# Kernel tuning notes

Measured on AMD Instinct MI355X. Metric: run time of the kernel, lower is better.

## Reference

```python
import jax, jax.numpy as jnp
import numpy as np
import math
from jax import lax

B, T, D, K, H, MLP_DIM, WIN = 4, 2048, 1024, 64, 4, 4096, 128
KH = K // H          # eigenstates per head
HD = D // H          # attention head dim


def layer_norm(x, g, b, eps=1e-5):
    mu = jnp.mean(x, axis=-1, keepdims=True)
    var = jnp.mean(jnp.square(x - mu), axis=-1, keepdims=True)
    return (x - mu) * lax.rsqrt(var + eps) * g + b


def setup_inputs() -> dict:
    key = jax.random.key(0)
    ks = jax.random.split(key, 16)
    s = 0.02
    # layer_idx=1, n_layers=6 -> depth_ratio=0.2, decay_center=-1.7
    return {
        "x": jax.random.normal(ks[0], (B, T, D), jnp.float32),
        "prev_eigenstates": jax.random.normal(ks[1], (B, T, 2 * K), jnp.float32),
        "norm1_g": jnp.ones((D,), jnp.float32),
        "norm1_b": jnp.zeros((D,), jnp.float32),
        "in_proj_w": jax.random.normal(ks[2], (2 * K, D), jnp.float32) * s,
        "memory_gate": jnp.array(-3.0, jnp.float32),
        "memory_proj_w": jnp.eye(2 * K, dtype=jnp.float32),
        "log_decay": jax.random.uniform(ks[3], (K,), jnp.float32, -2.7, -1.2),
        "frequency": jnp.linspace(0.0, 2 * math.pi * (1 - 1 / K), K, dtype=jnp.float32),
        "coupling": jnp.tile(jnp.eye(KH, dtype=jnp.float32), (H, 1, 1))
                    + 0.01 * jax.random.normal(ks[4], (H, KH, KH), jnp.float32) / math.sqrt(KH),
        "main_gate_w": jax.random.normal(ks[5], (D, D), jnp.float32) * s,
        "main_gate_b": jnp.full((D,), -2.0, jnp.float32),
        "out_proj_w": jax.random.normal(ks[6], (D, 2 * K), jnp.float32) * s,
        "attn_norm_g": jnp.ones((D,), jnp.float32),
        "attn_norm_b": jnp.zeros((D,), jnp.float32),
        "attn_in_w": jax.random.normal(ks[7], (3 * D, D), jnp.float32) * s,
        "attn_in_b": jnp.zeros((3 * D,), jnp.float32),
        "attn_out_w": jax.random.normal(ks[8], (D, D), jnp.float32) * s,
        "attn_out_b": jnp.zeros((D,), jnp.float32),
        "norm2_g": jnp.ones((D,), jnp.float32),
        "norm2_b": jnp.zeros((D,), jnp.float32),
        "mlp_w1": jax.random.normal(ks[9], (MLP_DIM, D), jnp.float32) * s,
        "mlp_b1": jnp.zeros((MLP_DIM,), jnp.float32),
        "mlp_w2": jax.random.normal(ks[10], (D, MLP_DIM), jnp.float32) * s,
        "mlp_b2": jnp.zeros((D,), jnp.float32),
    }


def eigenstate_fft(log_decay, frequency, beta_r, beta_i):
    # diagonal complex SSM recurrence: c_t = lam * c_{t-1} + beta_t
    lam = jnp.exp(log_decay)
    lr = lam * jnp.cos(frequency)   # (K,)
    li = lam * jnp.sin(frequency)
    br = jnp.transpose(beta_r, (1, 0, 2))  # (T,B,K)
    bi = jnp.transpose(beta_i, (1, 0, 2))

    def step(carry, inp):
        sr, si = carry
        xr, xi = inp
        nr = lr * sr - li * si + xr
        ni = lr * si + li * sr + xi
        return (nr, ni), (nr, ni)

    init = (jnp.zeros(br.shape[1:], br.dtype), jnp.zeros(bi.shape[1:], bi.dtype))
    _, (cr, ci) = lax.scan(step, init, (br, bi))
    return jnp.transpose(cr, (1, 0, 2)), jnp.transpose(ci, (1, 0, 2))


def reference(x, prev_eigenstates, norm1_g, norm1_b, in_proj_w, memory_gate,
              memory_proj_w, log_decay, frequency, coupling, main_gate_w,
              main_gate_b, out_proj_w, attn_norm_g, attn_norm_b, attn_in_w,
              attn_in_b, attn_out_w, attn_out_b, norm2_g, norm2_b,
              mlp_w1, mlp_b1, mlp_w2, mlp_b2):
    b, t, d = x.shape
    residual = x
    x_norm = layer_norm(x, norm1_g, norm1_b)

    beta = jnp.einsum('btd,kd->btk', x_norm, in_proj_w)        # (B,T,2K)
    beta_r, beta_i = jnp.split(beta, 2, axis=-1)

    # cross-layer memory
    mg = jax.nn.sigmoid(memory_gate)
    prev = jnp.einsum('btk,jk->btj', prev_eigenstates, memory_proj_w)
    pr, pi = jnp.split(prev, 2, axis=-1)
    beta_r = beta_r + mg * pr
    beta_i = beta_i + mg * pi

    c_r, c_i = eigenstate_fft(log_decay, frequency, beta_r, beta_i)  # (B,T,K)

    # per-head coupling
    c_r_h = c_r.reshape(b, t, H, KH)
    c_i_h = c_i.reshape(b, t, H, KH)
    c_r = jnp.einsum('hjk,bthk->bthj', coupling, c_r_h).reshape(b, t, K)
    c_i = jnp.einsum('hjk,bthk->bthj', coupling, c_i_h).reshape(b, t, K)
    eigenstates_out = jnp.concatenate([c_r, c_i], axis=-1)     # (B,T,2K)

    h = jnp.einsum('btk,dk->btd', eigenstates_out, out_proj_w)
    # spectral gate (band gates computed in torch are unused in the output)
    main_g = jax.nn.sigmoid(jnp.einsum('btd,ed->bte', x_norm, main_gate_w) + main_gate_b)
    h = main_g * h
    x = residual + h

    # sliding-window attention (dense masked MHA, as in the source)
    attn_in = layer_norm(x, attn_norm_g, attn_norm_b)
    qkv = jnp.einsum('btd,ed->bte', attn_in, attn_in_w) + attn_in_b
    q, k_, v = jnp.split(qkv, 3, axis=-1)
    q = q.reshape(b, t, H, HD).transpose(0, 2, 1, 3)           # (B,H,T,hd)
    k_ = k_.reshape(b, t, H, HD).transpose(0, 2, 1, 3)
    v = v.reshape(b, t, H, HD).transpose(0, 2, 1, 3)
    scale = 1.0 / math.sqrt(HD)
    scores = jnp.einsum('bhqd,bhkd->bhqk', q, k_) * scale
    idx = jnp.arange(t)
    diff = idx[:, None] - idx[None, :]
    allowed = (diff >= 0) & (diff <= WIN)                      # True = attend
    scores = jnp.where(allowed, scores, jnp.finfo(scores.dtype).min)
    attn = jax.nn.softmax(scores, axis=-1)
    ao = jnp.einsum('bhqk,bhkd->bhqd', attn, v)
    ao = ao.transpose(0, 2, 1, 3).reshape(b, t, d)
    ao = jnp.einsum('btd,ed->bte', ao, attn_out_w) + attn_out_b
    x = x + ao

    # MLP
    x2 = layer_norm(x, norm2_g, norm2_b)
    m = jax.nn.silu(jnp.einsum('btd,md->btm', x2, mlp_w1) + mlp_b1)
    m = jnp.einsum('btm,dm->btd', m, mlp_w2) + mlp_b2
    x = x + m
    return (x, eigenstates_out)
```

## Files before the change

### kernel.cpp

```cpp
#include <hip/hip_runtime.h>


typedef __bf16 bf16_t;
typedef bf16_t bf16x8 __attribute__((ext_vector_type(8)));
typedef bf16_t bf16x4 __attribute__((ext_vector_type(4)));
typedef float  f32x4  __attribute__((ext_vector_type(4)));

#define Tc   2048
#define Dc   1024
#define BTc  8192
#define K2c  128
#define MLPc 4096

struct ConvSeg { const float* src; bf16_t* dst; int n; };
struct ConvArgs { ConvSeg s[9]; };

__global__ __launch_bounds__(256) void convert_kernel(ConvArgs a) {
    ConvSeg sg = a.s[blockIdx.y];
    int i = (blockIdx.x * 256 + threadIdx.x) * 4;
    if (i >= sg.n) return;
    float4 v = *(const float4*)(sg.src + i);
    bf16x4 o;
    o[0] = (bf16_t)v.x; o[1] = (bf16_t)v.y; o[2] = (bf16_t)v.z; o[3] = (bf16_t)v.w;
    *(bf16x4*)(sg.dst + i) = o;
}

__global__ __launch_bounds__(256) void ln_kernel(const float* __restrict__ x,
                                                 const float* __restrict__ g,
                                                 const float* __restrict__ bb,
                                                 bf16_t* __restrict__ out) {
    int row = blockIdx.x;
    int tid = threadIdx.x;
    float4 v = ((const float4*)(x + (size_t)row * Dc))[tid];
    float s  = v.x + v.y + v.z + v.w;
    float ss = v.x * v.x + v.y * v.y + v.z * v.z + v.w * v.w;
#pragma unroll
    for (int d = 32; d > 0; d >>= 1) {
        s  += __shfl_down(s, d);
        ss += __shfl_down(ss, d);
    }
    __shared__ float red[8];
    int wv = tid >> 6;
    if ((tid & 63) == 0) { red[wv] = s; red[4 + wv] = ss; }
    __syncthreads();
    s  = red[0] + red[1] + red[2] + red[3];
    ss = red[4] + red[5] + red[6] + red[7];
    float mean = s * (1.0f / Dc);
    float var  = ss * (1.0f / Dc) - mean * mean;
    float rstd = rsqrtf(var + 1e-5f);
    float4 g4 = ((const float4*)g)[tid];
    float4 b4 = ((const float4*)bb)[tid];
    bf16x4 o;
    o[0] = (bf16_t)((v.x - mean) * rstd * g4.x + b4.x);
    o[1] = (bf16_t)((v.y - mean) * rstd * g4.y + b4.y);
    o[2] = (bf16_t)((v.z - mean) * rstd * g4.z + b4.z);
    o[3] = (bf16_t)((v.w - mean) * rstd * g4.w + b4.w);
    *(bf16x4*)(out + (size_t)row * Dc + tid * 4) = o;
}

#define BM 128
#define BN 128
#define BK 32

struct EpiParams {
    const float* bias;
    float*       fout;
    const float* fin;
    bf16_t*      bout;
    bf16_t*      q; bf16_t* k; bf16_t* v;
    const float* hbuf;
};

#define GLOAD_LDS(g, l)                                                        \
    __builtin_amdgcn_global_load_lds(                                          \
        (const __attribute__((address_space(1))) unsigned int*)(g),            \
        (__attribute__((address_space(3))) unsigned int*)(l), 16, 0, 0)

template <int EPI>
__global__ __launch_bounds__(256) void gemm_tiled(const bf16_t* __restrict__ A,
                                                  const bf16_t* __restrict__ W,
                                                  int M, int N, int K,
                                                  EpiParams ep) {
    __shared__ bf16_t As[BM * BK];
    __shared__ bf16_t Bs[BN * BK];

    int tid = threadIdx.x;
    int wv = tid >> 6, lane = tid & 63;
    int lane16 = lane & 15, quad = lane >> 4;
    int nbn = N / BN;
    int bm = blockIdx.x / nbn, bn = blockIdx.x % nbn;
    int m0 = bm * BM, n0 = bn * BN;
    int wm = (wv >> 1) * 64, wn = (wv & 1) * 64;

    int lrow = lane >> 2;
    int lcol = (lane & 3) * 8;
    const bf16_t* ga = A + (size_t)(m0 + wv * 16 + lrow) * K + lcol;
    const bf16_t* gb = W + (size_t)(n0 + wv * 16 + lrow) * K + lcol;
    size_t gstep64 = (size_t)64 * K;
    bf16_t* la0 = &As[(wv * 16) * BK];
    bf16_t* la1 = &As[(64 + wv * 16) * BK];
    bf16_t* lb0 = &Bs[(wv * 16) * BK];
    bf16_t* lb1 = &Bs[(64 + wv * 16) * BK];

    f32x4 zz = {0.f, 0.f, 0.f, 0.f};
    f32x4 acc[4][4];
#pragma unroll
    for (int mi = 0; mi < 4; mi++)
#pragma unroll
        for (int ni = 0; ni < 4; ni++) acc[mi][ni] = zz;

    for (int k0 = 0; k0 < K; k0 += BK) {
        GLOAD_LDS(ga + k0, la0);
        GLOAD_LDS(ga + k0 + gstep64, la1);
        GLOAD_LDS(gb + k0, lb0);
        GLOAD_LDS(gb + k0 + gstep64, lb1);
        __syncthreads();
        bf16x8 af[4], bf[4];
#pragma unroll
        for (int mi = 0; mi < 4; mi++)
            af[mi] = *(const bf16x8*)&As[(wm + mi * 16 + lane16) * BK + quad * 8];
#pragma unroll
        for (int ni = 0; ni < 4; ni++)
            bf[ni] = *(const bf16x8*)&Bs[(wn + ni * 16 + lane16) * BK + quad * 8];
#pragma unroll
        for (int mi = 0; mi < 4; mi++)
#pragma unroll
            for (int ni = 0; ni < 4; ni++)
                acc[mi][ni] = __builtin_amdgcn_mfma_f32_16x16x32_bf16(
                    af[mi], bf[ni], acc[mi][ni], 0, 0, 0);
        __syncthreads();
    }

#pragma unroll
    for (int mi = 0; mi < 4; mi++)
#pragma unroll
        for (int ni = 0; ni < 4; ni++)
#pragma unroll
            for (int r = 0; r < 4; r++) {
                int row = m0 + wm + mi * 16 + quad * 4 + r;
                int col = n0 + wn + ni * 16 + lane16;
                float v = acc[mi][ni][r];
                if constexpr (EPI == 0) {
                    ep.fout[(size_t)row * N + col] = v;
                } else if constexpr (EPI == 1) {
                    v += ep.bias[col];
                    ep.bout[(size_t)row * N + col] = (bf16_t)(v / (1.0f + __expf(-v)));
                } else if constexpr (EPI == 2) {
                    size_t o = (size_t)row * N + col;
                    ep.fout[o] = ep.fin[o] + v + ep.bias[col];
                } else if constexpr (EPI == 3) {
                    v += ep.bias[col];
                    int part = col >> 10, d1 = col & 1023;
                    int hh = d1 >> 8, hd = d1 & 255;
                    int b = row >> 11, t = row & 2047;
                    bf16_t* dst = (part == 0) ? ep.q : (part == 1) ? ep.k : ep.v;
                    dst[(((size_t)(b * 4 + hh) * Tc + t) << 8) + hd] = (bf16_t)v;
                } else if constexpr (EPI == 4) {
                    size_t o = (size_t)row * N + col;
                    float g = 1.0f / (1.0f + __expf(-(v + ep.bias[col])));
                    ep.fout[o] = ep.fin[o] + g * ep.hbuf[o];
                }
            }
}

__device__ __forceinline__ void mm32(const bf16_t* __restrict__ A,
                                     const bf16_t* __restrict__ W,
                                     int K, int m0, int n0,
                                     int lane16, int quad, f32x4 (&acc)[2][2]) {
    const bf16_t* a0 = A + (size_t)(m0 + lane16) * K + quad * 8;
    const bf16_t* a1 = a0 + (size_t)16 * K;
    const bf16_t* w0 = W + (size_t)(n0 + lane16) * K + quad * 8;
    const bf16_t* w1 = w0 + (size_t)16 * K;
#pragma unroll 4
    for (int k = 0; k < K; k += 32) {
        bf16x8 av0 = *(const bf16x8*)(a0 + k);
        bf16x8 av1 = *(const bf16x8*)(a1 + k);
        bf16x8 bv0 = *(const bf16x8*)(w0 + k);
        bf16x8 bv1 = *(const bf16x8*)(w1 + k);
        acc[0][0] = __builtin_amdgcn_mfma_f32_16x16x32_bf16(av0, bv0, acc[0][0], 0, 0, 0);
        acc[0][1] = __builtin_amdgcn_mfma_f32_16x16x32_bf16(av0, bv1, acc[0][1], 0, 0, 0);
        acc[1][0] = __builtin_amdgcn_mfma_f32_16x16x32_bf16(av1, bv0, acc[1][0], 0, 0, 0);
        acc[1][1] = __builtin_amdgcn_mfma_f32_16x16x32_bf16(av1, bv1, acc[1][1], 0, 0, 0);
    }
}

__global__ __launch_bounds__(256) void gemm_beta(const bf16_t* __restrict__ xn,
                                                 const bf16_t* __restrict__ ipw,
                                                 const bf16_t* __restrict__ prevb,
                                                 const bf16_t* __restrict__ mpw,
                                                 const float* __restrict__ mgate_p,
                                                 float* __restrict__ beta_c) {
    int lane = threadIdx.x & 63;
    int wave = threadIdx.x >> 6;
    int gid  = blockIdx.x * 4 + wave;
    int mt = gid / 4, nt = gid % 4;
    int m0 = mt * 32, n0 = nt * 32;
    int lane16 = lane & 15, quad = lane >> 4;
    f32x4 zz = {0.f, 0.f, 0.f, 0.f};
    f32x4 acc[2][2] = {{zz, zz}, {zz, zz}};
    mm32(xn, ipw, Dc, m0, n0, lane16, quad, acc);
    f32x4 acc2[2][2] = {{zz, zz}, {zz, zz}};
    mm32(prevb, mpw, K2c, m0, n0, lane16, quad, acc2);
    float mg = 1.0f / (1.0f + __expf(-mgate_p[0]));
    for (int mi = 0; mi < 2; mi++)
        for (int ni = 0; ni < 2; ni++)
            for (int r = 0; r < 4; r++) {
                int row = m0 + mi * 16 + quad * 4 + r;
                int col = n0 + ni * 16 + lane16;
                int b = row >> 11, t = row & 2047;
                beta_c[((size_t)b * K2c + col) * Tc + t] =
                    acc[mi][ni][r] + mg * acc2[mi][ni][r];
            }
}

__global__ __launch_bounds__(64) void scan_kernel(const float* __restrict__ beta_c,
                                                  const float* __restrict__ log_decay,
                                                  const float* __restrict__ freq,
                                                  float* __restrict__ cbuf) {
    int b = blockIdx.x >> 6;
    int k = blockIdx.x & 63;
    int lane = threadIdx.x;
    float lam = expf(log_decay[k]);
    float fr = freq[k];
    float lr = lam * cosf(fr), li = lam * sinf(fr);

    const float* br_p = beta_c + ((size_t)b * K2c + k) * Tc + lane * 32;
    const float* bi_p = beta_c + ((size_t)b * K2c + 64 + k) * Tc + lane * 32;
    float br[32], bi[32];
#pragma unroll
    for (int i = 0; i < 8; i++) {
        *(float4*)(&br[i * 4]) = ((const float4*)br_p)[i];
        *(float4*)(&bi[i * 4]) = ((const float4*)bi_p)[i];
    }
    float sr = 0.f, si = 0.f;
#pragma unroll
    for (int i = 0; i < 32; i++) {
        float nr = lr * sr - li * si + br[i];
        float ni = lr * si + li * sr + bi[i];
        sr = nr; si = ni;
    }
    float Mr = lr, Mi = li;
#pragma unroll
    for (int i = 0; i < 5; i++) {
        float nr = Mr * Mr - Mi * Mi, ni = 2.f * Mr * Mi;
        Mr = nr; Mi = ni;
    }
    float ir = sr, ii = si;
#pragma unroll
    for (int d = 1; d < 64; d <<= 1) {
        float pr = __shfl_up(ir, d);
        float pi = __shfl_up(ii, d);
        if (lane >= d) {
            ir += Mr * pr - Mi * pi;
            ii += Mr * pi + Mi * pr;
        }
        float nr = Mr * Mr - Mi * Mi, ni = 2.f * Mr * Mi;
        Mr = nr; Mi = ni;
    }
    float cr = __shfl_up(ir, 1), ci = __shfl_up(ii, 1);
    if (lane == 0) { cr = 0.f; ci = 0.f; }
    float* cr_p = cbuf + ((size_t)b * K2c + k) * Tc + lane * 32;
    float* ci_p = cbuf + ((size_t)b * K2c + 64 + k) * Tc + lane * 32;
    sr = cr; si = ci;
#pragma unroll
    for (int i = 0; i < 32; i++) {
        float nr = lr * sr - li * si + br[i];
        float ni = lr * si + li * sr + bi[i];
        sr = nr; si = ni;
        cr_p[i] = sr; ci_p[i] = si;
    }
}

__global__ __launch_bounds__(256) void coupling_kernel(const float* __restrict__ cbuf,
                                                       const float* __restrict__ cpl,
                                                       float* __restrict__ eig_out,
                                                       bf16_t* __restrict__ eigb) {
    int idx = blockIdx.x * 256 + threadIdx.x;
    int col = idx & 127;
    int t = (idx >> 7) & 2047;
    int b = idx >> 18;
    int ri = col >> 6, hj = col & 63, h2 = hj >> 4, j = hj & 15;
    const float* crow = cbuf + ((size_t)b * K2c + ri * 64 + h2 * 16) * Tc + t;
    const float* cw = cpl + (h2 * 16 + j) * 16;
    float acc = 0.f;
#pragma unroll
    for (int kk = 0; kk < 16; kk++) acc += cw[kk] * crow[(size_t)kk * Tc];
    eig_out[idx] = acc;
    eigb[idx] = (bf16_t)acc;
}

#define TQ   16
#define NK   144
#define LDQ  264
#define LDKV 136
#define LDS_S 161

__global__ __launch_bounds__(256) void attn_kernel(const bf16_t* __restrict__ qb,
                                                   const bf16_t* __restrict__ kb,
                                                   const bf16_t* __restrict__ vb,
                                                   bf16_t* __restrict__ ao) {
    __shared__ bf16_t Qs[TQ * LDQ];
    __shared__ bf16_t KVs[NK * LDKV];
    __shared__ float  S[TQ * LDS_S];
    __shared__ float  l_l[TQ];

    int tid = threadIdx.x;
    int qt = blockIdx.x & 127;
    int bh = blockIdx.x >> 7;
    int q0 = qt * TQ;
    const bf16_t* qp = qb + (size_t)bh * Tc * 256;
    const bf16_t* kp = kb + (size_t)bh * Tc * 256;
    const bf16_t* vp = vb + (size_t)bh * Tc * 256;

#pragma unroll
    for (int i = 0; i < 2; i++) {
        int lin = tid + i * 256;
        int row = lin >> 5, c = lin & 31;
        uint4 val = *(const uint4*)(qp + (size_t)(q0 + row) * 256 + c * 8);
        *(uint4*)(&Qs[row * LDQ + c * 8]) = val;
    }

    int q = tid >> 4;
    int kk0 = (tid & 15) * 9;
    float s9[9];
#pragma unroll
    for (int j = 0; j < 9; j++) s9[j] = 0.f;

    for (int ph = 0; ph < 2; ph++) {
        __syncthreads();
#pragma unroll
        for (int i = 0; i < 9; i++) {
            int lin = tid + i * 256;
            int row = lin >> 4, c = lin & 15;
            int kg = q0 - 128 + row;
            uint4 val = make_uint4(0u, 0u, 0u, 0u);
            if (kg >= 0) val = *(const uint4*)(kp + (size_t)kg * 256 + ph * 128 + c * 8);
            *(uint4*)(&KVs[row * LDKV + c * 8]) = val;
        }
        __syncthreads();
        for (int dt = 0; dt < 16; dt++) {
            float q8[8];
#pragma unroll
            for (int d = 0; d < 8; d++)
                q8[d] = (float)Qs[q * LDQ + ph * 128 + dt * 8 + d];
#pragma unroll
            for (int j = 0; j < 9; j++) {
                const bf16_t* kr = &KVs[(kk0 + j) * LDKV + dt * 8];
                float a = 0.f;
#pragma unroll
                for (int d = 0; d < 8; d++) a += q8[d] * (float)kr[d];
                s9[j] += a;
            }
        }
    }
#pragma unroll
    for (int j = 0; j < 9; j++) {
        int kk = kk0 + j;
        int kg = q0 - 128 + kk;
        bool ok = (kg >= 0) && (kk >= q) && (kk <= q + 128);
        S[q * LDS_S + kk] = ok ? s9[j] * 0.0625f : -1e30f;
    }
    __syncthreads();
    if (tid < TQ) {
        float m = -1e30f;
        for (int kk = 0; kk < NK; kk++) m = fmaxf(m, S[tid * LDS_S + kk]);
        float l = 0.f;
        for (int kk = 0; kk < NK; kk++) {
            float p = __expf(S[tid * LDS_S + kk] - m);
            S[tid * LDS_S + kk] = p;
            l += p;
        }
        l_l[tid] = l;
    }

    int dq = tid & 15;
    int b = bh >> 2, h = bh & 3;
    for (int ph = 0; ph < 2; ph++) {
        __syncthreads();
#pragma unroll
        for (int i = 0; i < 9; i++) {
            int lin = tid + i * 256;
            int row = lin >> 4, c = lin & 15;
            int kg = q0 - 128 + row;
            uint4 val = make_uint4(0u, 0u, 0u, 0u);
            if (kg >= 0) val = *(const uint4*)(vp + (size_t)kg * 256 + ph * 128 + c * 8);
            *(uint4*)(&KVs[row * LDKV + c * 8]) = val;
        }
        __syncthreads();
        float o[8];
#pragma unroll
        for (int j = 0; j < 8; j++) o[j] = 0.f;
        int d0 = dq * 8;
        for (int kk = 0; kk < NK; kk++) {
            float p = S[q * LDS_S + kk];
            const bf16_t* vr = &KVs[kk * LDKV + d0];
#pragma unroll
            for (int j = 0; j < 8; j++) o[j] += p * (float)vr[j];
        }
        float rl = 1.0f / l_l[q];
        bf16_t* dst = ao + ((size_t)(b * Tc + q0 + q)) * Dc + h * 256 + ph * 128 + d0;
#pragma unroll
        for (int j = 0; j < 8; j++) dst[j] = (bf16_t)(o[j] * rl);
    }
}

extern "C" void kernel_launch(void* const* d_in, const int* in_sizes, int n_in,
                              void* d_out, int out_size, void* d_ws, size_t ws_size,
                              hipStream_t stream) {
    const float* x            = (const float*)d_in[0];
    const float* prev_eig     = (const float*)d_in[1];
    const float* norm1_g      = (const float*)d_in[2];
    const float* norm1_b      = (const float*)d_in[3];
    const float* in_proj_w    = (const float*)d_in[4];
    const float* memory_gate  = (const float*)d_in[5];
    const float* memory_proj_w= (const float*)d_in[6];
    const float* log_decay    = (const float*)d_in[7];
    const float* frequency    = (const float*)d_in[8];
    const float* coupling     = (const float*)d_in[9];
    const float* main_gate_w  = (const float*)d_in[10];
    const float* main_gate_b  = (const float*)d_in[11];
    const float* out_proj_w   = (const float*)d_in[12];
    const float* attn_norm_g  = (const float*)d_in[13];
    const float* attn_norm_b  = (const float*)d_in[14];
    const float* attn_in_w    = (const float*)d_in[15];
    const float* attn_in_b    = (const float*)d_in[16];
    const float* attn_out_w   = (const float*)d_in[17];
    const float* attn_out_b   = (const float*)d_in[18];
    const float* norm2_g      = (const float*)d_in[19];
    const float* norm2_b      = (const float*)d_in[20];
    const float* mlp_w1       = (const float*)d_in[21];
    const float* mlp_b1       = (const float*)d_in[22];
    const float* mlp_w2       = (const float*)d_in[23];
    const float* mlp_b2       = (const float*)d_in[24];

    char* ws = (char*)d_ws;
    bf16_t* ipw_b  = (bf16_t*)(ws + 0);
    bf16_t* mpw_b  = (bf16_t*)(ws + 262144);
    bf16_t* mgw_b  = (bf16_t*)(ws + 294912);
    bf16_t* opw_b  = (bf16_t*)(ws + 2392064);
    bf16_t* aiw_b  = (bf16_t*)(ws + 2654208);
    bf16_t* aow_b  = (bf16_t*)(ws + 8945664);
    bf16_t* w1_b   = (bf16_t*)(ws + 11042816);
    bf16_t* w2_b   = (bf16_t*)(ws + 19431424);
    bf16_t* prev_b = (bf16_t*)(ws + 27820032);
    const size_t OFF_ACTA = 29917184;
    const size_t OFF_BIG  = OFF_ACTA + 16777216;
    bf16_t* actA   = (bf16_t*)(ws + OFF_ACTA);
    float*  beta_c = (float*)(ws + OFF_BIG);
    float*  cbuf   = (float*)(ws + OFF_BIG + 4194304);
    bf16_t* eigb   = (bf16_t*)(ws + OFF_BIG + 8388608);
    float*  hbuf   = (float*)(ws + OFF_BIG + 16777216);
    bf16_t* qbuf   = (bf16_t*)(ws + OFF_BIG);
    bf16_t* kbuf   = (bf16_t*)(ws + OFF_BIG + 16777216);
    bf16_t* vbuf   = (bf16_t*)(ws + OFF_BIG + 33554432);
    bf16_t* mbuf   = (bf16_t*)(ws + OFF_BIG);

    float* out_x   = (float*)d_out;
    float* out_eig = out_x + (size_t)BTc * Dc;
    float* xres    = out_x;

    ConvArgs ca;
    ca.s[0] = ConvSeg{in_proj_w,     ipw_b,  131072};
    ca.s[1] = ConvSeg{memory_proj_w, mpw_b,  16384};
    ca.s[2] = ConvSeg{main_gate_w,   mgw_b,  1048576};
    ca.s[3] = ConvSeg{out_proj_w,    opw_b,  131072};
    ca.s[4] = ConvSeg{attn_in_w,     aiw_b,  3145728};
    ca.s[5] = ConvSeg{attn_out_w,    aow_b,  1048576};
    ca.s[6] = ConvSeg{mlp_w1,        w1_b,   4194304};
    ca.s[7] = ConvSeg{mlp_w2,        w2_b,   4194304};
    ca.s[8] = ConvSeg{prev_eig,      prev_b, 1048576};
    convert_kernel<<<dim3(4096, 9), 256, 0, stream>>>(ca);

    EpiParams ep{};

    ln_kernel<<<BTc, 256, 0, stream>>>(x, norm1_g, norm1_b, actA);
    gemm_beta<<<256, 256, 0, stream>>>(actA, ipw_b, prev_b, mpw_b, memory_gate, beta_c);
    scan_kernel<<<256, 64, 0, stream>>>(beta_c, log_decay, frequency, cbuf);
    coupling_kernel<<<4096, 256, 0, stream>>>(cbuf, coupling, out_eig, eigb);
    ep = EpiParams{}; ep.fout = hbuf;
    gemm_tiled<0><<<(BTc/BM)*(Dc/BN), 256, 0, stream>>>(eigb, opw_b, BTc, Dc, K2c, ep);
    ep = EpiParams{}; ep.bias = main_gate_b; ep.fin = x; ep.fout = xres; ep.hbuf = hbuf;
    gemm_tiled<4><<<(BTc/BM)*(Dc/BN), 256, 0, stream>>>(actA, mgw_b, BTc, Dc, Dc, ep);
    ln_kernel<<<BTc, 256, 0, stream>>>(xres, attn_norm_g, attn_norm_b, actA);
    ep = EpiParams{}; ep.bias = attn_in_b; ep.q = qbuf; ep.k = kbuf; ep.v = vbuf;
    gemm_tiled<3><<<(BTc/BM)*(3*Dc/BN), 256, 0, stream>>>(actA, aiw_b, BTc, 3*Dc, Dc, ep);
    attn_kernel<<<2048, 256, 0, stream>>>(qbuf, kbuf, vbuf, actA);
    ep = EpiParams{}; ep.bias = attn_out_b; ep.fin = xres; ep.fout = xres;
    gemm_tiled<2><<<(BTc/BM)*(Dc/BN), 256, 0, stream>>>(actA, aow_b, BTc, Dc, Dc, ep);
    ln_kernel<<<BTc, 256, 0, stream>>>(xres, norm2_g, norm2_b, actA);
    ep = EpiParams{}; ep.bias = mlp_b1; ep.bout = mbuf;
    gemm_tiled<1><<<(BTc/BM)*(MLPc/BN), 256, 0, stream>>>(actA, w1_b, BTc, MLPc, Dc, ep);
    ep = EpiParams{}; ep.bias = mlp_b2; ep.fin = xres; ep.fout = out_x;
    gemm_tiled<2><<<(BTc/BM)*(Dc/BN), 256, 0, stream>>>(mbuf, w2_b, BTc, Dc, MLPc, ep);

    (void)in_sizes; (void)n_in; (void)out_size; (void)ws_size;
}
```

Baseline: 799.5 us.

## Rewrite sliding-window attention with MFMA and produce transposed V via swapped GEMM

The scalar-FMA attention kernel is replaced by an MFMA kernel in which each wave handles 16 queries. It computes QK^T over a 144-key window with MFMA, does the softmax in registers using shuffles, and stages P in LDS for the PV MFMA. To feed PV, the QKV projection is split: Q/K keep the original epilogue, while V is computed by a swapped-operand GEMM (weights × activations) whose new epilogue writes V transposed (per head: dim × T). This removes the slow scalar dot products and LDS round trips. The cost is an extra GEMM launch, and K/V fragments are read directly from global memory with no LDS staging.

```diff
diff --git a/kernel.cpp b/kernel.cpp
--- a/kernel.cpp
+++ b/kernel.cpp
@@ -115,19 +115,19 @@
         GLOAD_LDS(gb + k0, lb0);
         GLOAD_LDS(gb + k0 + gstep64, lb1);
         __syncthreads();
-        bf16x8 af[4], bf[4];
+        bf16x8 af[4], bfr[4];
 #pragma unroll
         for (int mi = 0; mi < 4; mi++)
             af[mi] = *(const bf16x8*)&As[(wm + mi * 16 + lane16) * BK + quad * 8];
 #pragma unroll
         for (int ni = 0; ni < 4; ni++)
-            bf[ni] = *(const bf16x8*)&Bs[(wn + ni * 16 + lane16) * BK + quad * 8];
+            bfr[ni] = *(const bf16x8*)&Bs[(wn + ni * 16 + lane16) * BK + quad * 8];
 #pragma unroll
         for (int mi = 0; mi < 4; mi++)
 #pragma unroll
             for (int ni = 0; ni < 4; ni++)
                 acc[mi][ni] = __builtin_amdgcn_mfma_f32_16x16x32_bf16(
-                    af[mi], bf[ni], acc[mi][ni], 0, 0, 0);
+                    af[mi], bfr[ni], acc[mi][ni], 0, 0, 0);
         __syncthreads();
     }
 
@@ -153,12 +153,17 @@
                     int part = col >> 10, d1 = col & 1023;
                     int hh = d1 >> 8, hd = d1 & 255;
                     int b = row >> 11, t = row & 2047;
-                    bf16_t* dst = (part == 0) ? ep.q : (part == 1) ? ep.k : ep.v;
+                    bf16_t* dst = (part == 0) ? ep.q : ep.k;
                     dst[(((size_t)(b * 4 + hh) * Tc + t) << 8) + hd] = (bf16_t)v;
                 } else if constexpr (EPI == 4) {
                     size_t o = (size_t)row * N + col;
                     float g = 1.0f / (1.0f + __expf(-(v + ep.bias[col])));
                     ep.fout[o] = ep.fin[o] + g * ep.hbuf[o];
+                } else if constexpr (EPI == 5) {
+                    v += ep.bias[2048 + row];
+                    int b = col >> 11, t = col & 2047;
+                    int hh = row >> 8, dd = row & 255;
+                    ep.v[((size_t)((b * 4 + hh) * 256 + dd)) * Tc + t] = (bf16_t)v;
                 }
             }
 }
@@ -289,119 +294,125 @@
     eigb[idx] = (bf16_t)acc;
 }
 
-#define TQ   16
-#define NK   144
-#define LDQ  264
-#define LDKV 136
-#define LDS_S 161
-
-__global__ __launch_bounds__(256) void attn_kernel(const bf16_t* __restrict__ qb,
-                                                   const bf16_t* __restrict__ kb,
-                                                   const bf16_t* __restrict__ vb,
-                                                   bf16_t* __restrict__ ao) {
-    __shared__ bf16_t Qs[TQ * LDQ];
-    __shared__ bf16_t KVs[NK * LDKV];
-    __shared__ float  S[TQ * LDS_S];
-    __shared__ float  l_l[TQ];
-
+#define LDP 168
+
+__global__ __launch_bounds__(256) void attn_mfma(const bf16_t* __restrict__ qb,
+                                                 const bf16_t* __restrict__ kb,
+                                                 const bf16_t* __restrict__ vt,
+                                                 bf16_t* __restrict__ ao) {
+    __shared__ bf16_t Pl[4 * 16 * LDP];
     int tid = threadIdx.x;
-    int qt = blockIdx.x & 127;
-    int bh = blockIdx.x >> 7;
-    int q0 = qt * TQ;
+    int wv = tid >> 6, lane = tid & 63;
+    int lane16 = lane & 15, quad = lane >> 4;
+    int qblk = blockIdx.x & 31;
+    int bh = blockIdx.x >> 5;
+    int qw0 = qblk * 64 + wv * 16;
     const bf16_t* qp = qb + (size_t)bh * Tc * 256;
     const bf16_t* kp = kb + (size_t)bh * Tc * 256;
-    const bf16_t* vp = vb + (size_t)bh * Tc * 256;
-
-#pragma unroll
-    for (int i = 0; i < 2; i++) {
-        int lin = tid + i * 256;
-        int row = lin >> 5, c = lin & 31;
-        uint4 val = *(const uint4*)(qp + (size_t)(q0 + row) * 256 + c * 8);
-        *(uint4*)(&Qs[row * LDQ + c * 8]) = val;
-    }
-
-    int q = tid >> 4;
-    int kk0 = (tid & 15) * 9;
-    float s9[9];
-#pragma unroll
-    for (int j = 0; j < 9; j++) s9[j] = 0.f;
-
-    for (int ph = 0; ph < 2; ph++) {
-        __syncthreads();
-#pragma unroll
-        for (int i = 0; i < 9; i++) {
-            int lin = tid + i * 256;
-            int row = lin >> 4, c = lin & 15;
-            int kg = q0 - 128 + row;
-            uint4 val = make_uint4(0u, 0u, 0u, 0u);
-            if (kg >= 0) val = *(const uint4*)(kp + (size_t)kg * 256 + ph * 128 + c * 8);
-            *(uint4*)(&KVs[row * LDKV + c * 8]) = val;
+    const bf16_t* vp = vt + (size_t)bh * 256 * Tc;
+    bf16_t* Pw = &Pl[wv * 16 * LDP];
+
+    for (int i = lane; i < 16 * 24; i += 64) {
+        int r = i / 24, c = 144 + (i % 24);
+        Pw[r * LDP + c] = (bf16_t)0.f;
+    }
+
+    bf16x8 qf[8];
+#pragma unroll
+    for (int ks = 0; ks < 8; ks++)
+        qf[ks] = *(const bf16x8*)(qp + (size_t)(qw0 + lane16) * 256 + ks * 32 + quad * 8);
+
+    f32x4 zz = {0.f, 0.f, 0.f, 0.f};
+    f32x4 S[9];
+#pragma unroll
+    for (int jt = 0; jt < 9; jt++) S[jt] = zz;
+    int kbase = qw0 - 128;
+
+#pragma unroll
+    for (int ks = 0; ks < 8; ks++) {
+        bf16x8 kf[9];
+#pragma unroll
+        for (int jt = 0; jt < 9; jt++) {
+            int krow = kbase + jt * 16 + lane16;
+            krow = krow < 0 ? 0 : krow;
+            kf[jt] = *(const bf16x8*)(kp + (size_t)krow * 256 + ks * 32 + quad * 8);
         }
-        __syncthreads();
-        for (int dt = 0; dt < 16; dt++) {
-            float q8[8];
-#pragma unroll
-            for (int d = 0; d < 8; d++)
-                q8[d] = (float)Qs[q * LDQ + ph * 128 + dt * 8 + d];
-#pragma unroll
-            for (int j = 0; j < 9; j++) {
-                const bf16_t* kr = &KVs[(kk0 + j) * LDKV + dt * 8];
-                float a = 0.f;
-#pragma unroll
-                for (int d = 0; d < 8; d++) a += q8[d] * (float)kr[d];
-                s9[j] += a;
-            }
+#pragma unroll
+        for (int jt = 0; jt < 9; jt++)
+            S[jt] = __builtin_amdgcn_mfma_f32_16x16x32_bf16(qf[ks], kf[jt], S[jt], 0, 0, 0);
+    }
+
+    float m[4], l[4];
+#pragma unroll
+    for (int r = 0; r < 4; r++) m[r] = -1e30f;
+#pragma unroll
+    for (int jt = 0; jt < 9; jt++) {
+        int kg = kbase + jt * 16 + lane16;
+#pragma unroll
+        for (int r = 0; r < 4; r++) {
+            int qrow = qw0 + quad * 4 + r;
+            bool ok = (kg >= 0) && (kg <= qrow) && (kg >= qrow - 128);
+            float v = ok ? S[jt][r] * 0.0625f : -1e30f;
+            S[jt][r] = v;
+            m[r] = fmaxf(m[r], v);
         }
     }
 #pragma unroll
-    for (int j = 0; j < 9; j++) {
-        int kk = kk0 + j;
-        int kg = q0 - 128 + kk;
-        bool ok = (kg >= 0) && (kk >= q) && (kk <= q + 128);
-        S[q * LDS_S + kk] = ok ? s9[j] * 0.0625f : -1e30f;
-    }
+    for (int d = 1; d < 16; d <<= 1)
+#pragma unroll
+        for (int r = 0; r < 4; r++)
+            m[r] = fmaxf(m[r], __shfl_xor(m[r], d));
+#pragma unroll
+    for (int r = 0; r < 4; r++) l[r] = 0.f;
+#pragma unroll
+    for (int jt = 0; jt < 9; jt++)
+#pragma unroll
+        for (int r = 0; r < 4; r++) {
+            float p = __expf(S[jt][r] - m[r]);
+            S[jt][r] = p;
+            l[r] += p;
+        }
+#pragma unroll
+    for (int d = 1; d < 16; d <<= 1)
+#pragma unroll
+        for (int r = 0; r < 4; r++)
+            l[r] += __shfl_xor(l[r], d);
+
+#pragma unroll
+    for (int jt = 0; jt < 9; jt++)
+#pragma unroll
+        for (int r = 0; r < 4; r++)
+            Pw[(quad * 4 + r) * LDP + jt * 16 + lane16] = (bf16_t)S[jt][r];
     __syncthreads();
-    if (tid < TQ) {
-        float m = -1e30f;
-        for (int kk = 0; kk < NK; kk++) m = fmaxf(m, S[tid * LDS_S + kk]);
-        float l = 0.f;
-        for (int kk = 0; kk < NK; kk++) {
-            float p = __expf(S[tid * LDS_S + kk] - m);
-            S[tid * LDS_S + kk] = p;
-            l += p;
+
+    f32x4 O[16];
+#pragma unroll
+    for (int nt = 0; nt < 16; nt++) O[nt] = zz;
+#pragma unroll
+    for (int ks = 0; ks < 5; ks++) {
+        bf16x8 pf = *(const bf16x8*)&Pw[lane16 * LDP + ks * 32 + quad * 8];
+        int kidx = kbase + ks * 32 + quad * 8;
+        kidx = kidx < 0 ? 0 : kidx;
+        kidx = kidx > (Tc - 8) ? (Tc - 8) : kidx;
+#pragma unroll
+        for (int nt = 0; nt < 16; nt++) {
+            bf16x8 vf = *(const bf16x8*)(vp + (size_t)(nt * 16 + lane16) * Tc + kidx);
+            O[nt] = __builtin_amdgcn_mfma_f32_16x16x32_bf16(pf, vf, O[nt], 0, 0, 0);
         }
-        l_l[tid] = l;
-    }
-
-    int dq = tid & 15;
+    }
+
+    float rl[4];
+#pragma unroll
+    for (int r = 0; r < 4; r++) rl[r] = 1.0f / l[r];
     int b = bh >> 2, h = bh & 3;
-    for (int ph = 0; ph < 2; ph++) {
-        __syncthreads();
-#pragma unroll
-        for (int i = 0; i < 9; i++) {
-            int lin = tid + i * 256;
-            int row = lin >> 4, c = lin & 15;
-            int kg = q0 - 128 + row;
-            uint4 val = make_uint4(0u, 0u, 0u, 0u);
-            if (kg >= 0) val = *(const uint4*)(vp + (size_t)kg * 256 + ph * 128 + c * 8);
-            *(uint4*)(&KVs[row * LDKV + c * 8]) = val;
+#pragma unroll
+    for (int nt = 0; nt < 16; nt++)
+#pragma unroll
+        for (int r = 0; r < 4; r++) {
+            int qrow = qw0 + quad * 4 + r;
+            int dim = nt * 16 + lane16;
+            ao[((size_t)(b * Tc + qrow)) * Dc + h * 256 + dim] = (bf16_t)(O[nt][r] * rl[r]);
         }
-        __syncthreads();
-        float o[8];
-#pragma unroll
-        for (int j = 0; j < 8; j++) o[j] = 0.f;
-        int d0 = dq * 8;
-        for (int kk = 0; kk < NK; kk++) {
-            float p = S[q * LDS_S + kk];
-            const bf16_t* vr = &KVs[kk * LDKV + d0];
-#pragma unroll
-            for (int j = 0; j < 8; j++) o[j] += p * (float)vr[j];
-        }
-        float rl = 1.0f / l_l[q];
-        bf16_t* dst = ao + ((size_t)(b * Tc + q0 + q)) * Dc + h * 256 + ph * 128 + d0;
-#pragma unroll
-        for (int j = 0; j < 8; j++) dst[j] = (bf16_t)(o[j] * rl);
-    }
 }
 
 extern "C" void kernel_launch(void* const* d_in, const int* in_sizes, int n_in,
@@ -452,7 +463,7 @@
     float*  hbuf   = (float*)(ws + OFF_BIG + 16777216);
     bf16_t* qbuf   = (bf16_t*)(ws + OFF_BIG);
     bf16_t* kbuf   = (bf16_t*)(ws + OFF_BIG + 16777216);
-    bf16_t* vbuf   = (bf16_t*)(ws + OFF_BIG + 33554432);
+    bf16_t* vtbuf  = (bf16_t*)(ws + OFF_BIG + 33554432);
     bf16_t* mbuf   = (bf16_t*)(ws + OFF_BIG);
 
     float* out_x   = (float*)d_out;
@@ -482,9 +493,12 @@
     ep = EpiParams{}; ep.bias = main_gate_b; ep.fin = x; ep.fout = xres; ep.hbuf = hbuf;
     gemm_tiled<4><<<(BTc/BM)*(Dc/BN), 256, 0, stream>>>(actA, mgw_b, BTc, Dc, Dc, ep);
     ln_kernel<<<BTc, 256, 0, stream>>>(xres, attn_norm_g, attn_norm_b, actA);
-    ep = EpiParams{}; ep.bias = attn_in_b; ep.q = qbuf; ep.k = kbuf; ep.v = vbuf;
-    gemm_tiled<3><<<(BTc/BM)*(3*Dc/BN), 256, 0, stream>>>(actA, aiw_b, BTc, 3*Dc, Dc, ep);
-    attn_kernel<<<2048, 256, 0, stream>>>(qbuf, kbuf, vbuf, actA);
+    ep = EpiParams{}; ep.bias = attn_in_b; ep.q = qbuf; ep.k = kbuf;
+    gemm_tiled<3><<<(BTc/BM)*(2048/BN), 256, 0, stream>>>(actA, aiw_b, BTc, 2048, Dc, ep);
+    ep = EpiParams{}; ep.bias = attn_in_b; ep.v = vtbuf;
+    gemm_tiled<5><<<(Dc/BM)*(BTc/BN), 256, 0, stream>>>(aiw_b + (size_t)2048 * Dc, actA,
+                                                        Dc, BTc, Dc, ep);
+    attn_mfma<<<512, 256, 0, stream>>>(qbuf, kbuf, vtbuf, actA);
     ep = EpiParams{}; ep.bias = attn_out_b; ep.fin = xres; ep.fout = xres;
     gemm_tiled<2><<<(BTc/BM)*(Dc/BN), 256, 0, stream>>>(actA, aow_b, BTc, Dc, Dc, ep);
     ln_kernel<<<BTc, 256, 0, stream>>>(xres, norm2_g, norm2_b, actA);
```

Result: faster. 695.1 us (-13.1%).
